# Optimization experiments

Hardware: AMD Instinct MI355X
Metric: run time of the kernel (lower is better)

## Reference

```python
import jax, jax.numpy as jnp
import numpy as np

NUM_GENES = 9229
NUM_FEATURES = 3
BATCH = 4096


def setup_inputs() -> dict:
    key = jax.random.key(0)
    k1, k2, k3 = jax.random.split(key, 3)
    x = jax.random.normal(k1, (BATCH, NUM_GENES * NUM_FEATURES), dtype=jnp.float32)
    weights = jax.random.normal(k2, (NUM_GENES * NUM_FEATURES,), dtype=jnp.float32)
    bias = 0.1 * jax.random.normal(k3, (NUM_GENES,), dtype=jnp.float32)
    return {"x": x, "weights": weights, "bias": bias}


def reference(x, weights, bias):
    # Block-diagonal scatter + mm is equivalent to a per-gene weighted sum
    # over the feature dimension:
    # x: [B, G*F] -> [B, G, F]; weights: [G*F] -> [G, F]
    B = x.shape[0]
    xg = x.reshape(B, NUM_GENES, NUM_FEATURES)
    wg = weights.reshape(NUM_GENES, NUM_FEATURES)
    out = jnp.einsum("bgf,gf->bg", xg, wg) + bias  # [B, G]
    return out
```

## Files before the change

### kernel.cpp

```cpp
#include <hip/hip_runtime.h>


#define G    9229
#define GF   27687
#define B    4096
#define GB   2308
#define BLK  256
#define GBG  10
#define RPC  16
#define NRC  (B / RPC)

__global__ __launch_bounds__(BLK) void diag_layer_kernel(
    const float* __restrict__ x,
    const float* __restrict__ w,
    const float* __restrict__ bias,
    float* __restrict__ out) {

    const int t   = threadIdx.x;
    const int gbg = (int)blockIdx.x % GBG;
    const int rc  = (int)blockIdx.x / GBG;
    const int gb  = gbg * BLK + t;
    if (gb >= GB) return;

    const int row0 = rc * RPC;

    if (gb < GB - 1) {
        const float4 w0 = *reinterpret_cast<const float4*>(w + 12 * gb);
        const float4 w1 = *reinterpret_cast<const float4*>(w + 12 * gb + 4);
        const float4 w2 = *reinterpret_cast<const float4*>(w + 12 * gb + 8);
        const float4 bv = *reinterpret_cast<const float4*>(bias + 4 * gb);

#pragma unroll 4
        for (int r = 0; r < RPC; ++r) {
            const unsigned b  = (unsigned)(row0 + r);
            const unsigned xb = b * (unsigned)GF + 12u * (unsigned)gb;
            const float4 v0 = *reinterpret_cast<const float4*>(x + xb);
            const float4 v1 = *reinterpret_cast<const float4*>(x + xb + 4);
            const float4 v2 = *reinterpret_cast<const float4*>(x + xb + 8);
            float4 o;
            o.x = fmaf(v0.x, w0.x, fmaf(v0.y, w0.y, fmaf(v0.z, w0.z, bv.x)));
            o.y = fmaf(v0.w, w0.w, fmaf(v1.x, w1.x, fmaf(v1.y, w1.y, bv.y)));
            o.z = fmaf(v1.z, w1.z, fmaf(v1.w, w1.w, fmaf(v2.x, w2.x, bv.z)));
            o.w = fmaf(v2.y, w2.y, fmaf(v2.z, w2.z, fmaf(v2.w, w2.w, bv.w)));
            *reinterpret_cast<float4*>(out + (size_t)b * G + 4u * (unsigned)gb) = o;
        }
    } else {
        const float wa = w[3 * (G - 1)];
        const float wb_ = w[3 * (G - 1) + 1];
        const float wc = w[3 * (G - 1) + 2];
        const float bz = bias[G - 1];
        for (int r = 0; r < RPC; ++r) {
            const unsigned b  = (unsigned)(row0 + r);
            const unsigned xb = b * (unsigned)GF + 3u * (G - 1);
            out[(size_t)b * G + (G - 1)] =
                fmaf(x[xb], wa, fmaf(x[xb + 1], wb_, fmaf(x[xb + 2], wc, bz)));
        }
    }
}

extern "C" void kernel_launch(void* const* d_in, const int* in_sizes, int n_in,
                              void* d_out, int out_size, void* d_ws, size_t ws_size,
                              hipStream_t stream) {
    const float* x    = (const float*)d_in[0];
    const float* w    = (const float*)d_in[1];
    const float* bias = (const float*)d_in[2];
    float* out        = (float*)d_out;

    diag_layer_kernel<<<GBG * NRC, BLK, 0, stream>>>(x, w, bias, out);
}
```

Baseline: 146.8 us.

## Use grid-stride persistent blocks over smaller 4-row work units

The kernel now launches a fixed grid of 2048 blocks that loop over 10240 work units, each covering 256 gene groups by 4 batch rows, instead of one block per 16-row chunk. Unit ordering puts the row index in the low bits, so concurrently running blocks share the same gene-group columns and therefore the same weights. The goal is to reduce launch and tail overhead and to improve load balance and memory-level parallelism for this bandwidth-bound kernel. In exchange, each unit reloads weights more often and fully unrolls only 4 rows, which leaves fewer loads in flight per thread.

```diff
diff --git a/kernel.cpp b/kernel.cpp
--- a/kernel.cpp
+++ b/kernel.cpp
@@ -1,14 +1,12 @@
 #include <hip/hip_runtime.h>
 
 
-#define G    9229
-#define GF   27687
-#define B    4096
-#define GB   2308
-#define BLK  256
-#define GBG  10
-#define RPC  16
-#define NRC  (B / RPC)
+#define G     9229
+#define GF    27687
+#define B     4096
+#define BLK   256
+#define GRID  2048
+#define NUNIT 10240
 
 __global__ __launch_bounds__(BLK) void diag_layer_kernel(
     const float* __restrict__ x,
@@ -16,44 +14,46 @@
     const float* __restrict__ bias,
     float* __restrict__ out) {
 
-    const int t   = threadIdx.x;
-    const int gbg = (int)blockIdx.x % GBG;
-    const int rc  = (int)blockIdx.x / GBG;
-    const int gb  = gbg * BLK + t;
-    if (gb >= GB) return;
+    const int t = threadIdx.x;
 
-    const int row0 = rc * RPC;
+    for (int u = (int)blockIdx.x; u < NUNIT; u += GRID) {
+        const int gbg  = u >> 10;
+        const int rc   = u & 1023;
+        const int gb   = gbg * BLK + t;
+        const int row0 = rc * 4;
 
-    if (gb < GB - 1) {
-        const float4 w0 = *reinterpret_cast<const float4*>(w + 12 * gb);
-        const float4 w1 = *reinterpret_cast<const float4*>(w + 12 * gb + 4);
-        const float4 w2 = *reinterpret_cast<const float4*>(w + 12 * gb + 8);
-        const float4 bv = *reinterpret_cast<const float4*>(bias + 4 * gb);
+        if (gb < 2307) {
+            const float4 w0 = *reinterpret_cast<const float4*>(w + 12 * gb);
+            const float4 w1 = *reinterpret_cast<const float4*>(w + 12 * gb + 4);
+            const float4 w2 = *reinterpret_cast<const float4*>(w + 12 * gb + 8);
+            const float4 bv = *reinterpret_cast<const float4*>(bias + 4 * gb);
 
-#pragma unroll 4
-        for (int r = 0; r < RPC; ++r) {
-            const unsigned b  = (unsigned)(row0 + r);
-            const unsigned xb = b * (unsigned)GF + 12u * (unsigned)gb;
-            const float4 v0 = *reinterpret_cast<const float4*>(x + xb);
-            const float4 v1 = *reinterpret_cast<const float4*>(x + xb + 4);
-            const float4 v2 = *reinterpret_cast<const float4*>(x + xb + 8);
-            float4 o;
-            o.x = fmaf(v0.x, w0.x, fmaf(v0.y, w0.y, fmaf(v0.z, w0.z, bv.x)));
-            o.y = fmaf(v0.w, w0.w, fmaf(v1.x, w1.x, fmaf(v1.y, w1.y, bv.y)));
-            o.z = fmaf(v1.z, w1.z, fmaf(v1.w, w1.w, fmaf(v2.x, w2.x, bv.z)));
-            o.w = fmaf(v2.y, w2.y, fmaf(v2.z, w2.z, fmaf(v2.w, w2.w, bv.w)));
-            *reinterpret_cast<float4*>(out + (size_t)b * G + 4u * (unsigned)gb) = o;
-        }
-    } else {
-        const float wa = w[3 * (G - 1)];
-        const float wb_ = w[3 * (G - 1) + 1];
-        const float wc = w[3 * (G - 1) + 2];
-        const float bz = bias[G - 1];
-        for (int r = 0; r < RPC; ++r) {
-            const unsigned b  = (unsigned)(row0 + r);
-            const unsigned xb = b * (unsigned)GF + 3u * (G - 1);
-            out[(size_t)b * G + (G - 1)] =
-                fmaf(x[xb], wa, fmaf(x[xb + 1], wb_, fmaf(x[xb + 2], wc, bz)));
+#pragma unroll
+            for (int r = 0; r < 4; ++r) {
+                const unsigned b  = (unsigned)(row0 + r);
+                const unsigned xb = b * (unsigned)GF + 12u * (unsigned)gb;
+                const float4 v0 = *reinterpret_cast<const float4*>(x + xb);
+                const float4 v1 = *reinterpret_cast<const float4*>(x + xb + 4);
+                const float4 v2 = *reinterpret_cast<const float4*>(x + xb + 8);
+                float4 o;
+                o.x = fmaf(v0.x, w0.x, fmaf(v0.y, w0.y, fmaf(v0.z, w0.z, bv.x)));
+                o.y = fmaf(v0.w, w0.w, fmaf(v1.x, w1.x, fmaf(v1.y, w1.y, bv.y)));
+                o.z = fmaf(v1.z, w1.z, fmaf(v1.w, w1.w, fmaf(v2.x, w2.x, bv.z)));
+                o.w = fmaf(v2.y, w2.y, fmaf(v2.z, w2.z, fmaf(v2.w, w2.w, bv.w)));
+                *reinterpret_cast<float4*>(out + b * (unsigned)G + 4u * (unsigned)gb) = o;
+            }
+        } else if (gb == 2307) {
+            const float wa = w[3 * (G - 1)];
+            const float wb_ = w[3 * (G - 1) + 1];
+            const float wc = w[3 * (G - 1) + 2];
+            const float bz = bias[G - 1];
+#pragma unroll
+            for (int r = 0; r < 4; ++r) {
+                const unsigned b  = (unsigned)(row0 + r);
+                const unsigned xb = b * (unsigned)GF + 3u * (G - 1);
+                out[b * (unsigned)G + (G - 1)] =
+                    fmaf(x[xb], wa, fmaf(x[xb + 1], wb_, fmaf(x[xb + 2], wc, bz)));
+            }
         }
     }
 }
@@ -66,5 +66,5 @@
     const float* bias = (const float*)d_in[2];
     float* out        = (float*)d_out;
 
-    diag_layer_kernel<<<GBG * NRC, BLK, 0, stream>>>(x, w, bias, out);
+    diag_layer_kernel<<<GRID, BLK, 0, stream>>>(x, w, bias, out);
 }
```

Result: faster. 129.5 us (-11.8%).
